# Performance work log

Hardware: AMD Instinct MI355X
Metric: run time of the kernel (lower is better)

Reference implementation:

```python
import jax, jax.numpy as jnp
import numpy as np

IN_DIM = 1024
OUT_DIM = 128
N = 8192


def setup_inputs() -> dict:
    key = jax.random.key(0)
    ks = jax.random.split(key, 7)
    s = 1.0 / np.sqrt(IN_DIM)
    return {
        "z": jax.random.normal(ks[0], (N, IN_DIM), dtype=jnp.float32),
        "Wq": jax.random.normal(ks[1], (IN_DIM, OUT_DIM), dtype=jnp.float32) * s,
        "bq": jax.random.normal(ks[2], (OUT_DIM,), dtype=jnp.float32) * 0.01,
        "Wk": jax.random.normal(ks[3], (IN_DIM, OUT_DIM), dtype=jnp.float32) * s,
        "bk": jax.random.normal(ks[4], (OUT_DIM,), dtype=jnp.float32) * 0.01,
        "Wv": jax.random.normal(ks[5], (IN_DIM, OUT_DIM), dtype=jnp.float32) * s,
        "bv": jax.random.normal(ks[6], (OUT_DIM,), dtype=jnp.float32) * 0.01,
    }


def reference(z, Wq, bq, Wk, bk, Wv, bv):
    # QKV projections: [N, in_dim] @ [in_dim, out_dim] + bias -> [N, out_dim]
    q = z @ Wq + bq
    k = z @ Wk + bk
    v = z @ Wv + bv
    dh = q.shape[-1]
    # Scores [N, N], scaled by sqrt(dh); softmax over last axis (torch 2-D default)
    scores = (q @ k.T) * (1.0 / jnp.sqrt(jnp.asarray(dh, q.dtype)))
    A = jax.nn.softmax(scores, axis=-1)
    return A @ v
```

## Files before the change

kernel.cpp:

```cpp
#include <hip/hip_runtime.h>


#define N_TOK   8192
#define D_IN    1024
#define D_HEAD  128
#define SCALE   0.08838834764831845f
#define SPLIT   4

typedef _Float16 half8 __attribute__((ext_vector_type(8)));
typedef _Float16 half4 __attribute__((ext_vector_type(4)));
typedef float f32x4 __attribute__((ext_vector_type(4)));

__global__ void prep_wt(const float* __restrict__ Wq, const float* __restrict__ Wk,
                        const float* __restrict__ Wv, _Float16* __restrict__ Wt) {
    int i = blockIdx.x * 256 + threadIdx.x;
    int mat = i >> 17;
    int rem = i & 131071;
    int n = rem >> 10;
    int c = rem & 1023;
    const float* W = (mat == 0) ? Wq : (mat == 1) ? Wk : Wv;
    float v = W[c * 128 + n];
    if (mat == 0) v *= SCALE;
    Wt[i] = (_Float16)v;
}

__launch_bounds__(256)
__global__ void qkv_gemm(const float* __restrict__ z, const _Float16* __restrict__ Wt,
                         const float* __restrict__ bq, const float* __restrict__ bk,
                         const float* __restrict__ bv,
                         _Float16* __restrict__ Qs, _Float16* __restrict__ Kh,
                         _Float16* __restrict__ Vt) {
    __shared__ __align__(16) _Float16 A_lds[64 * 72];
    __shared__ __align__(16) _Float16 B_lds[128 * 72];
    const int mat = blockIdx.y;
    const int m0 = blockIdx.x * 64;
    const int t = threadIdx.x;
    const int lane = t & 63, w = t >> 6;
    const int l15 = lane & 15, g = lane >> 4;
    const _Float16* Wm = Wt + (size_t)mat * 131072;

    f32x4 acc[8] = {};

    const int arow = t >> 2, aseg = t & 3;
    const int bn = t >> 1, bh = t & 1;

    for (int c0 = 0; c0 < D_IN; c0 += 64) {
        const float4* zp = reinterpret_cast<const float4*>(
            z + (size_t)(m0 + arow) * D_IN + c0 + aseg * 16);
        float4 f0 = zp[0], f1 = zp[1], f2 = zp[2], f3 = zp[3];
        const half8* wp = reinterpret_cast<const half8*>(Wm + (size_t)bn * D_IN + c0 + bh * 32);
        half8 w0 = wp[0], w1 = wp[1], w2 = wp[2], w3 = wp[3];

        __syncthreads();

        half8 h0, h1;
        h0[0]=(_Float16)f0.x; h0[1]=(_Float16)f0.y; h0[2]=(_Float16)f0.z; h0[3]=(_Float16)f0.w;
        h0[4]=(_Float16)f1.x; h0[5]=(_Float16)f1.y; h0[6]=(_Float16)f1.z; h0[7]=(_Float16)f1.w;
        h1[0]=(_Float16)f2.x; h1[1]=(_Float16)f2.y; h1[2]=(_Float16)f2.z; h1[3]=(_Float16)f2.w;
        h1[4]=(_Float16)f3.x; h1[5]=(_Float16)f3.y; h1[6]=(_Float16)f3.z; h1[7]=(_Float16)f3.w;
        *reinterpret_cast<half8*>(&A_lds[arow * 72 + aseg * 16])     = h0;
        *reinterpret_cast<half8*>(&A_lds[arow * 72 + aseg * 16 + 8]) = h1;
        half8* bd = reinterpret_cast<half8*>(&B_lds[bn * 72 + bh * 32]);
        bd[0] = w0; bd[1] = w1; bd[2] = w2; bd[3] = w3;

        __syncthreads();

        half8 a0 = *reinterpret_cast<half8*>(&A_lds[(w * 16 + l15) * 72 + g * 8]);
        half8 a1 = *reinterpret_cast<half8*>(&A_lds[(w * 16 + l15) * 72 + 32 + g * 8]);
#pragma unroll
        for (int nt = 0; nt < 8; nt++) {
            half8 b0 = *reinterpret_cast<half8*>(&B_lds[(nt * 16 + l15) * 72 + g * 8]);
            half8 b1 = *reinterpret_cast<half8*>(&B_lds[(nt * 16 + l15) * 72 + 32 + g * 8]);
            acc[nt] = __builtin_amdgcn_mfma_f32_16x16x32_f16(a0, b0, acc[nt], 0, 0, 0);
            acc[nt] = __builtin_amdgcn_mfma_f32_16x16x32_f16(a1, b1, acc[nt], 0, 0, 0);
        }
    }

    const float* bias = (mat == 0) ? bq : (mat == 1) ? bk : bv;
    if (mat < 2) {
        _Float16* dst = (mat == 0) ? Qs : Kh;
#pragma unroll
        for (int nt = 0; nt < 8; nt++) {
            float b = bias[nt * 16 + l15];
            if (mat == 0) b *= SCALE;
#pragma unroll
            for (int r = 0; r < 4; r++) {
                int m = m0 + w * 16 + g * 4 + r;
                dst[(size_t)m * D_HEAD + nt * 16 + l15] = (_Float16)(acc[nt][r] + b);
            }
        }
    } else {
#pragma unroll
        for (int nt = 0; nt < 8; nt++) {
            float b = bias[nt * 16 + l15];
            half4 pk;
#pragma unroll
            for (int r = 0; r < 4; r++) pk[r] = (_Float16)(acc[nt][r] + b);
            int m = m0 + w * 16 + g * 4;
            *reinterpret_cast<half4*>(&Vt[(size_t)(nt * 16 + l15) * N_TOK + m]) = pk;
        }
    }
}

__launch_bounds__(256)
__global__ void attn(const _Float16* __restrict__ Qs, const _Float16* __restrict__ Kh,
                     const _Float16* __restrict__ Vt,
                     float* __restrict__ Opart, float* __restrict__ lpart) {
    __shared__ __align__(16) _Float16 K_lds[64 * 136];
    __shared__ __align__(16) _Float16 V_lds[128 * 72];
    __shared__ __align__(16) _Float16 P_lds[64 * 72];

    const int t = threadIdx.x;
    const int lane = t & 63, w = t >> 6;
    const int l15 = lane & 15, g = lane >> 4;
    const int q0 = blockIdx.x * 64;
    const int sp = blockIdx.y;
    const int kvA = sp * (N_TOK / SPLIT), kvB = kvA + N_TOK / SPLIT;

    half8 qa[4];
    {
        const _Float16* qrow = Qs + (size_t)(q0 + w * 16 + l15) * D_HEAD + g * 8;
#pragma unroll
        for (int ct = 0; ct < 4; ct++)
            qa[ct] = *reinterpret_cast<const half8*>(qrow + ct * 32);
    }

    f32x4 o[8] = {};
    float lsum[4] = {0.f, 0.f, 0.f, 0.f};

    const int krow = t >> 2, kseg = t & 3;
    const int vd = t >> 1, vh = t & 1;

    for (int kv = kvA; kv < kvB; kv += 64) {
        const half8* kp = reinterpret_cast<const half8*>(
            Kh + (size_t)(kv + krow) * D_HEAD + kseg * 32);
        half8 k0 = kp[0], k1 = kp[1], k2 = kp[2], k3 = kp[3];
        const half8* vp = reinterpret_cast<const half8*>(
            Vt + (size_t)vd * N_TOK + kv + vh * 32);
        half8 v0 = vp[0], v1 = vp[1], v2 = vp[2], v3 = vp[3];

        __syncthreads();

        half8* kd = reinterpret_cast<half8*>(&K_lds[krow * 136 + kseg * 32]);
        kd[0] = k0; kd[1] = k1; kd[2] = k2; kd[3] = k3;
        half8* vdp = reinterpret_cast<half8*>(&V_lds[vd * 72 + vh * 32]);
        vdp[0] = v0; vdp[1] = v1; vdp[2] = v2; vdp[3] = v3;

        __syncthreads();

        f32x4 sf[4];
#pragma unroll
        for (int kt = 0; kt < 4; kt++) {
            f32x4 s4 = {0.f, 0.f, 0.f, 0.f};
#pragma unroll
            for (int ct = 0; ct < 4; ct++) {
                half8 kf = *reinterpret_cast<half8*>(
                    &K_lds[(kt * 16 + l15) * 136 + ct * 32 + g * 8]);
                s4 = __builtin_amdgcn_mfma_f32_16x16x32_f16(qa[ct], kf, s4, 0, 0, 0);
            }
            sf[kt] = s4;
        }

#pragma unroll
        for (int kt = 0; kt < 4; kt++) {
#pragma unroll
            for (int r = 0; r < 4; r++) {
                float p = __expf(sf[kt][r]);
                lsum[r] += p;
                P_lds[(w * 16 + g * 4 + r) * 72 + kt * 16 + l15] = (_Float16)p;
            }
        }

        half8 pf0 = *reinterpret_cast<half8*>(&P_lds[(w * 16 + l15) * 72 + g * 8]);
        half8 pf1 = *reinterpret_cast<half8*>(&P_lds[(w * 16 + l15) * 72 + 32 + g * 8]);
#pragma unroll
        for (int dt = 0; dt < 8; dt++) {
            half8 vf0 = *reinterpret_cast<half8*>(&V_lds[(dt * 16 + l15) * 72 + g * 8]);
            half8 vf1 = *reinterpret_cast<half8*>(&V_lds[(dt * 16 + l15) * 72 + 32 + g * 8]);
            o[dt] = __builtin_amdgcn_mfma_f32_16x16x32_f16(pf0, vf0, o[dt], 0, 0, 0);
            o[dt] = __builtin_amdgcn_mfma_f32_16x16x32_f16(pf1, vf1, o[dt], 0, 0, 0);
        }
    }

#pragma unroll
    for (int r = 0; r < 4; r++) {
        float v = lsum[r];
        v += __shfl_xor(v, 1, 64);
        v += __shfl_xor(v, 2, 64);
        v += __shfl_xor(v, 4, 64);
        v += __shfl_xor(v, 8, 64);
        lsum[r] = v;
    }

    float* Op = Opart + (size_t)sp * N_TOK * D_HEAD;
#pragma unroll
    for (int dt = 0; dt < 8; dt++)
#pragma unroll
        for (int r = 0; r < 4; r++)
            Op[(size_t)(q0 + w * 16 + g * 4 + r) * D_HEAD + dt * 16 + l15] = o[dt][r];
    if (l15 == 0) {
#pragma unroll
        for (int r = 0; r < 4; r++)
            lpart[sp * N_TOK + q0 + w * 16 + g * 4 + r] = lsum[r];
    }
}

__global__ void combine(const float* __restrict__ Opart, const float* __restrict__ lpart,
                        float* __restrict__ out) {
    int i = blockIdx.x * 256 + threadIdx.x;
    int m = i >> 7;
    float num = 0.f, den = 0.f;
#pragma unroll
    for (int s = 0; s < SPLIT; s++) {
        num += Opart[(size_t)s * N_TOK * D_HEAD + i];
        den += lpart[s * N_TOK + m];
    }
    out[i] = num / den;
}

extern "C" void kernel_launch(void* const* d_in, const int* in_sizes, int n_in,
                              void* d_out, int out_size, void* d_ws, size_t ws_size,
                              hipStream_t stream) {
    const float* z  = (const float*)d_in[0];
    const float* Wq = (const float*)d_in[1];
    const float* bq = (const float*)d_in[2];
    const float* Wk = (const float*)d_in[3];
    const float* bk = (const float*)d_in[4];
    const float* Wv = (const float*)d_in[5];
    const float* bv = (const float*)d_in[6];
    float* out = (float*)d_out;

    char* ws = (char*)d_ws;
    _Float16* Wt = (_Float16*)(ws);
    _Float16* Qs = (_Float16*)(ws + 786432);
    _Float16* Kh = (_Float16*)(ws + 786432 + 2097152);
    _Float16* Vt = (_Float16*)(ws + 786432 + 2 * 2097152);
    float* Opart = (float*)(ws + 786432 + 3 * 2097152);
    float* lpart = (float*)(ws + 786432 + 3 * 2097152 + (size_t)SPLIT * N_TOK * D_HEAD * 4);

    prep_wt<<<1536, 256, 0, stream>>>(Wq, Wk, Wv, Wt);
    qkv_gemm<<<dim3(128, 3), 256, 0, stream>>>(z, Wt, bq, bk, bv, Qs, Kh, Vt);
    attn<<<dim3(128, SPLIT), 256, 0, stream>>>(Qs, Kh, Vt, Opart, lpart);
    combine<<<4096, 256, 0, stream>>>(Opart, lpart, out);
}
```

Baseline: 183.0 us.

## Restructure attention kernel with 128-row Q tiles, swizzled LDS, prefetch, fp16 partials

The attention kernel now handles 128 query rows per block, two 16-row tiles per wave, so each K/V fragment read from LDS feeds twice as many MFMAs. It also moves to an XOR-swizzled LDS layout in place of padding, prefetches the next K/V tile into registers, and uses exp2 with log2e folded into the Q scale. Further changes raise SPLIT to 8, add s_setprio and launch bounds for two blocks per CU, and store the partial outputs as fp16 with a vectorized combine. Together these aim to cut LDS traffic, hide global latency and shrink partial-output bandwidth, at the cost of more registers and fp16 rounding of the unnormalized partial sums.

Measured after the change: 149.6 us. -18.2%, faster.

```diff
diff --git a/kernel.cpp b/kernel.cpp
--- a/kernel.cpp
+++ b/kernel.cpp
@@ -4,8 +4,11 @@
 #define N_TOK   8192
 #define D_IN    1024
 #define D_HEAD  128
-#define SCALE   0.08838834764831845f
-#define SPLIT   4
+#define QSCALE  (0.08838834764831845f * 1.4426950408889634f)
+#define SPLIT   8
+#define QB      128
+#define KVB     64
+#define NIT     ((N_TOK / SPLIT) / KVB)
 
 typedef _Float16 half8 __attribute__((ext_vector_type(8)));
 typedef _Float16 half4 __attribute__((ext_vector_type(4)));
@@ -20,7 +23,7 @@
     int c = rem & 1023;
     const float* W = (mat == 0) ? Wq : (mat == 1) ? Wk : Wv;
     float v = W[c * 128 + n];
-    if (mat == 0) v *= SCALE;
+    if (mat == 0) v *= QSCALE;
     Wt[i] = (_Float16)v;
 }
 
@@ -82,7 +85,7 @@
 #pragma unroll
         for (int nt = 0; nt < 8; nt++) {
             float b = bias[nt * 16 + l15];
-            if (mat == 0) b *= SCALE;
+            if (mat == 0) b *= QSCALE;
 #pragma unroll
             for (int r = 0; r < 4; r++) {
                 int m = m0 + w * 16 + g * 4 + r;
@@ -102,120 +105,178 @@
     }
 }
 
-__launch_bounds__(256)
+__launch_bounds__(256, 2)
 __global__ void attn(const _Float16* __restrict__ Qs, const _Float16* __restrict__ Kh,
                      const _Float16* __restrict__ Vt,
-                     float* __restrict__ Opart, float* __restrict__ lpart) {
-    __shared__ __align__(16) _Float16 K_lds[64 * 136];
-    __shared__ __align__(16) _Float16 V_lds[128 * 72];
-    __shared__ __align__(16) _Float16 P_lds[64 * 72];
+                     _Float16* __restrict__ Opart, float* __restrict__ lpart) {
+    __shared__ __align__(16) char lds[49152];
+    char* Kb = lds;
+    char* Vb = lds + 16384;
+    char* Pb = lds + 32768;
 
     const int t = threadIdx.x;
     const int lane = t & 63, w = t >> 6;
     const int l15 = lane & 15, g = lane >> 4;
-    const int q0 = blockIdx.x * 64;
+    const int q0 = blockIdx.x * QB;
     const int sp = blockIdx.y;
-    const int kvA = sp * (N_TOK / SPLIT), kvB = kvA + N_TOK / SPLIT;
-
-    half8 qa[4];
-    {
-        const _Float16* qrow = Qs + (size_t)(q0 + w * 16 + l15) * D_HEAD + g * 8;
+    const int kvA = sp * (N_TOK / SPLIT);
+
+    half8 qa[2][4];
+#pragma unroll
+    for (int r16 = 0; r16 < 2; r16++)
 #pragma unroll
         for (int ct = 0; ct < 4; ct++)
-            qa[ct] = *reinterpret_cast<const half8*>(qrow + ct * 32);
-    }
-
-    f32x4 o[8] = {};
-    float lsum[4] = {0.f, 0.f, 0.f, 0.f};
+            qa[r16][ct] = *reinterpret_cast<const half8*>(
+                Qs + (size_t)(q0 + w * 32 + r16 * 16 + l15) * D_HEAD + ct * 32 + g * 8);
 
     const int krow = t >> 2, kseg = t & 3;
     const int vd = t >> 1, vh = t & 1;
-
-    for (int kv = kvA; kv < kvB; kv += 64) {
-        const half8* kp = reinterpret_cast<const half8*>(
-            Kh + (size_t)(kv + krow) * D_HEAD + kseg * 32);
-        half8 k0 = kp[0], k1 = kp[1], k2 = kp[2], k3 = kp[3];
-        const half8* vp = reinterpret_cast<const half8*>(
-            Vt + (size_t)vd * N_TOK + kv + vh * 32);
-        half8 v0 = vp[0], v1 = vp[1], v2 = vp[2], v3 = vp[3];
-
+    int kw[4], vw[4];
+#pragma unroll
+    for (int i = 0; i < 4; i++) {
+        kw[i] = krow * 256 + (((kseg * 4 + i) ^ (krow & 7)) << 4);
+        vw[i] = vd * 128 + (((vh * 4 + i) ^ (vd & 7)) << 4);
+    }
+    int kru[4], vru[2];
+#pragma unroll
+    for (int ct = 0; ct < 4; ct++) kru[ct] = ((ct * 4 + g) ^ (l15 & 7)) << 4;
+#pragma unroll
+    for (int s2 = 0; s2 < 2; s2++) vru[s2] = ((s2 * 4 + g) ^ (l15 & 7)) << 4;
+    char* Pw = Pb + w * 4096;
+    const int phi = l15 >> 3, plo = (l15 & 7) * 2;
+    int px[4];
+#pragma unroll
+    for (int r = 0; r < 4; r++) px[r] = (g * 4 + r) & 7;
+
+    f32x4 o[2][8] = {};
+    float lsum[2][4] = {};
+
+    const _Float16* kg = Kh + (size_t)(kvA + krow) * D_HEAD + kseg * 32;
+    const _Float16* vg = Vt + (size_t)vd * N_TOK + kvA + vh * 32;
+    half8 kr[4], vr[4];
+#pragma unroll
+    for (int i = 0; i < 4; i++) {
+        kr[i] = reinterpret_cast<const half8*>(kg)[i];
+        vr[i] = reinterpret_cast<const half8*>(vg)[i];
+    }
+
+    for (int it = 0; it < NIT; ++it) {
         __syncthreads();
-
-        half8* kd = reinterpret_cast<half8*>(&K_lds[krow * 136 + kseg * 32]);
-        kd[0] = k0; kd[1] = k1; kd[2] = k2; kd[3] = k3;
-        half8* vdp = reinterpret_cast<half8*>(&V_lds[vd * 72 + vh * 32]);
-        vdp[0] = v0; vdp[1] = v1; vdp[2] = v2; vdp[3] = v3;
-
+#pragma unroll
+        for (int i = 0; i < 4; i++) {
+            *reinterpret_cast<half8*>(Kb + kw[i]) = kr[i];
+            *reinterpret_cast<half8*>(Vb + vw[i]) = vr[i];
+        }
         __syncthreads();
 
-        f32x4 sf[4];
+        if (it + 1 < NIT) {
+            kg += (size_t)KVB * D_HEAD;
+            vg += KVB;
+#pragma unroll
+            for (int i = 0; i < 4; i++) {
+                kr[i] = reinterpret_cast<const half8*>(kg)[i];
+                vr[i] = reinterpret_cast<const half8*>(vg)[i];
+            }
+        }
+
+        f32x4 sf[2][4] = {};
+        __builtin_amdgcn_s_setprio(1);
 #pragma unroll
         for (int kt = 0; kt < 4; kt++) {
-            f32x4 s4 = {0.f, 0.f, 0.f, 0.f};
 #pragma unroll
             for (int ct = 0; ct < 4; ct++) {
-                half8 kf = *reinterpret_cast<half8*>(
-                    &K_lds[(kt * 16 + l15) * 136 + ct * 32 + g * 8]);
-                s4 = __builtin_amdgcn_mfma_f32_16x16x32_f16(qa[ct], kf, s4, 0, 0, 0);
+                half8 kf = *reinterpret_cast<half8*>(Kb + kt * 4096 + l15 * 256 + kru[ct]);
+#pragma unroll
+                for (int r16 = 0; r16 < 2; r16++)
+                    sf[r16][kt] = __builtin_amdgcn_mfma_f32_16x16x32_f16(
+                        qa[r16][ct], kf, sf[r16][kt], 0, 0, 0);
             }
-            sf[kt] = s4;
-        }
-
-#pragma unroll
-        for (int kt = 0; kt < 4; kt++) {
-#pragma unroll
-            for (int r = 0; r < 4; r++) {
-                float p = __expf(sf[kt][r]);
-                lsum[r] += p;
-                P_lds[(w * 16 + g * 4 + r) * 72 + kt * 16 + l15] = (_Float16)p;
+        }
+        __builtin_amdgcn_s_setprio(0);
+
+#pragma unroll
+        for (int r16 = 0; r16 < 2; r16++)
+#pragma unroll
+            for (int kt = 0; kt < 4; kt++)
+#pragma unroll
+                for (int r = 0; r < 4; r++) {
+                    float p = __builtin_amdgcn_exp2f(sf[r16][kt][r]);
+                    lsum[r16][r] += p;
+                    *reinterpret_cast<_Float16*>(
+                        Pw + r16 * 2048 + (g * 4 + r) * 128 +
+                        (((kt * 2 + phi) ^ px[r]) << 4) + plo) = (_Float16)p;
+                }
+
+        __builtin_amdgcn_s_setprio(1);
+#pragma unroll
+        for (int s2 = 0; s2 < 2; s2++) {
+            half8 pa[2];
+#pragma unroll
+            for (int r16 = 0; r16 < 2; r16++)
+                pa[r16] = *reinterpret_cast<half8*>(Pw + r16 * 2048 + l15 * 128 + vru[s2]);
+#pragma unroll
+            for (int dt = 0; dt < 8; dt++) {
+                half8 vf = *reinterpret_cast<half8*>(Vb + dt * 2048 + l15 * 128 + vru[s2]);
+#pragma unroll
+                for (int r16 = 0; r16 < 2; r16++)
+                    o[r16][dt] = __builtin_amdgcn_mfma_f32_16x16x32_f16(
+                        pa[r16], vf, o[r16][dt], 0, 0, 0);
             }
         }
-
-        half8 pf0 = *reinterpret_cast<half8*>(&P_lds[(w * 16 + l15) * 72 + g * 8]);
-        half8 pf1 = *reinterpret_cast<half8*>(&P_lds[(w * 16 + l15) * 72 + 32 + g * 8]);
-#pragma unroll
-        for (int dt = 0; dt < 8; dt++) {
-            half8 vf0 = *reinterpret_cast<half8*>(&V_lds[(dt * 16 + l15) * 72 + g * 8]);
-            half8 vf1 = *reinterpret_cast<half8*>(&V_lds[(dt * 16 + l15) * 72 + 32 + g * 8]);
-            o[dt] = __builtin_amdgcn_mfma_f32_16x16x32_f16(pf0, vf0, o[dt], 0, 0, 0);
-            o[dt] = __builtin_amdgcn_mfma_f32_16x16x32_f16(pf1, vf1, o[dt], 0, 0, 0);
-        }
-    }
-
-#pragma unroll
-    for (int r = 0; r < 4; r++) {
-        float v = lsum[r];
-        v += __shfl_xor(v, 1, 64);
-        v += __shfl_xor(v, 2, 64);
-        v += __shfl_xor(v, 4, 64);
-        v += __shfl_xor(v, 8, 64);
-        lsum[r] = v;
-    }
-
-    float* Op = Opart + (size_t)sp * N_TOK * D_HEAD;
-#pragma unroll
-    for (int dt = 0; dt < 8; dt++)
-#pragma unroll
-        for (int r = 0; r < 4; r++)
-            Op[(size_t)(q0 + w * 16 + g * 4 + r) * D_HEAD + dt * 16 + l15] = o[dt][r];
+        __builtin_amdgcn_s_setprio(0);
+    }
+
+#pragma unroll
+    for (int r16 = 0; r16 < 2; r16++)
+#pragma unroll
+        for (int r = 0; r < 4; r++) {
+            float v = lsum[r16][r];
+            v += __shfl_xor(v, 1, 64);
+            v += __shfl_xor(v, 2, 64);
+            v += __shfl_xor(v, 4, 64);
+            v += __shfl_xor(v, 8, 64);
+            lsum[r16][r] = v;
+        }
+
+    _Float16* Op = Opart + (size_t)sp * N_TOK * D_HEAD;
+#pragma unroll
+    for (int r16 = 0; r16 < 2; r16++)
+#pragma unroll
+        for (int dt = 0; dt < 8; dt++)
+#pragma unroll
+            for (int r = 0; r < 4; r++)
+                Op[(size_t)(q0 + w * 32 + r16 * 16 + g * 4 + r) * D_HEAD + dt * 16 + l15] =
+                    (_Float16)o[r16][dt][r];
     if (l15 == 0) {
 #pragma unroll
-        for (int r = 0; r < 4; r++)
-            lpart[sp * N_TOK + q0 + w * 16 + g * 4 + r] = lsum[r];
-    }
-}
-
-__global__ void combine(const float* __restrict__ Opart, const float* __restrict__ lpart,
+        for (int r16 = 0; r16 < 2; r16++)
+#pragma unroll
+            for (int r = 0; r < 4; r++)
+                lpart[sp * N_TOK + q0 + w * 32 + r16 * 16 + g * 4 + r] = lsum[r16][r];
+    }
+}
+
+__global__ void combine(const _Float16* __restrict__ Opart, const float* __restrict__ lpart,
                         float* __restrict__ out) {
     int i = blockIdx.x * 256 + threadIdx.x;
-    int m = i >> 7;
-    float num = 0.f, den = 0.f;
+    int base = i * 8;
+    int m = base >> 7;
+    float acc[8] = {};
+    float den = 0.f;
 #pragma unroll
     for (int s = 0; s < SPLIT; s++) {
-        num += Opart[(size_t)s * N_TOK * D_HEAD + i];
+        half8 h = *reinterpret_cast<const half8*>(
+            Opart + (size_t)s * N_TOK * D_HEAD + base);
+#pragma unroll
+        for (int j = 0; j < 8; j++) acc[j] += (float)h[j];
         den += lpart[s * N_TOK + m];
     }
-    out[i] = num / den;
+    float inv = 1.f / den;
+    float4 o0, o1;
+    o0.x = acc[0]*inv; o0.y = acc[1]*inv; o0.z = acc[2]*inv; o0.w = acc[3]*inv;
+    o1.x = acc[4]*inv; o1.y = acc[5]*inv; o1.z = acc[6]*inv; o1.w = acc[7]*inv;
+    reinterpret_cast<float4*>(out + base)[0] = o0;
+    reinterpret_cast<float4*>(out + base)[1] = o1;
 }
 
 extern "C" void kernel_launch(void* const* d_in, const int* in_sizes, int n_in,
@@ -235,11 +296,12 @@
     _Float16* Qs = (_Float16*)(ws + 786432);
     _Float16* Kh = (_Float16*)(ws + 786432 + 2097152);
     _Float16* Vt = (_Float16*)(ws + 786432 + 2 * 2097152);
-    float* Opart = (float*)(ws + 786432 + 3 * 2097152);
-    float* lpart = (float*)(ws + 786432 + 3 * 2097152 + (size_t)SPLIT * N_TOK * D_HEAD * 4);
+    _Float16* Opart = (_Float16*)(ws + 786432 + 3 * 2097152);
+    float* lpart = (float*)(ws + 786432 + 3 * 2097152 +
+                            (size_t)SPLIT * N_TOK * D_HEAD * 2);
 
     prep_wt<<<1536, 256, 0, stream>>>(Wq, Wk, Wv, Wt);
     qkv_gemm<<<dim3(128, 3), 256, 0, stream>>>(z, Wt, bq, bk, bv, Qs, Kh, Vt);
-    attn<<<dim3(128, SPLIT), 256, 0, stream>>>(Qs, Kh, Vt, Opart, lpart);
-    combine<<<4096, 256, 0, stream>>>(Opart, lpart, out);
-}
+    attn<<<dim3(N_TOK / QB, SPLIT), 256, 0, stream>>>(Qs, Kh, Vt, Opart, lpart);
+    combine<<<512, 256, 0, stream>>>(Opart, lpart, out);
+}
```
